# Performance work log

Hardware: AMD Instinct MI355X
Metric: run time of the kernel (lower is better)

## Reference

```python
import jax, jax.numpy as jnp
import numpy as np

N = 100000
E = 1600000
B = 64
EPS = 1e-5


def setup_inputs() -> dict:
    key = jax.random.key(0)
    ks = jax.random.split(key, 20)
    x = jax.random.normal(ks[0], (N, 3), dtype=jnp.float32)
    edge_index = jax.random.randint(ks[1], (2, E), 0, N, dtype=jnp.int64)
    batch = jnp.sort(jax.random.randint(ks[2], (N,), 0, B, dtype=jnp.int64))

    def lin(k, fan_in, fan_out):
        s = 1.0 / np.sqrt(fan_in)
        kw, kb = jax.random.split(k)
        W = jax.random.uniform(kw, (fan_in, fan_out), minval=-s, maxval=s, dtype=jnp.float32)
        b = jax.random.uniform(kb, (fan_out,), minval=-s, maxval=s, dtype=jnp.float32)
        return W, b

    W1, b1 = lin(ks[3], 3, 16)
    W2, b2 = lin(ks[4], 16, 32)
    W3, b3 = lin(ks[5], 32, 64)
    fcW, fcb = lin(ks[6], 64, 10)
    g1 = jnp.ones((16,), jnp.float32); be1 = jnp.zeros((16,), jnp.float32)
    g2 = jnp.ones((32,), jnp.float32); be2 = jnp.zeros((32,), jnp.float32)
    g3 = jnp.ones((64,), jnp.float32); be3 = jnp.zeros((64,), jnp.float32)
    return {"x": x, "edge_index": edge_index, "batch": batch,
            "W1": W1, "b1": b1, "g1": g1, "be1": be1,
            "W2": W2, "b2": b2, "g2": g2, "be2": be2,
            "W3": W3, "b3": b3, "g3": g3, "be3": be3,
            "fcW": fcW, "fcb": fcb}


def _gcn_conv(x, W, b, row, col, deg_inv_sqrt):
    # PyG GCNConv: add self-loops (pre-appended in row/col), symmetric norm,
    # scatter-add aggregation at target nodes, then bias.
    xw = x @ W                                   # [N, d_out]
    norm = deg_inv_sqrt[row] * deg_inv_sqrt[col]  # [E+N]
    msg = xw[row] * norm[:, None]                 # gather + scale
    out = jax.ops.segment_sum(msg, col, num_segments=N)
    return out + b


def _bn_relu(x, gamma, beta):
    mean = jnp.mean(x, axis=0)
    var = jnp.mean(jnp.square(x - mean), axis=0)  # biased var (torch BN)
    xh = (x - mean) * jax.lax.rsqrt(var + EPS)
    return jax.nn.relu(xh * gamma + beta)


def reference(x, edge_index, batch, W1, b1, g1, be1, W2, b2, g2, be2,
              W3, b3, g3, be3, fcW, fcb):
    loops = jnp.arange(N, dtype=edge_index.dtype)
    row = jnp.concatenate([edge_index[0], loops])
    col = jnp.concatenate([edge_index[1], loops])
    deg = jax.ops.segment_sum(jnp.ones_like(col, dtype=x.dtype), col, num_segments=N)
    dis = jax.lax.rsqrt(deg)  # deg >= 1 due to self-loops

    h = _bn_relu(_gcn_conv(x, W1, b1, row, col, dis), g1, be1)
    h = _bn_relu(_gcn_conv(h, W2, b2, row, col, dis), g2, be2)
    h = _bn_relu(_gcn_conv(h, W3, b3, row, col, dis), g3, be3)

    sums = jax.ops.segment_sum(h, batch, num_segments=B)          # [B, 64]
    cnts = jax.ops.segment_sum(jnp.ones((N,), h.dtype), batch, num_segments=B)
    pooled = sums / jnp.maximum(cnts, 1.0)[:, None]
    return pooled @ fcW + fcb                                     # [B, 10]
```

## Files before the change

### kernel.cpp

```cpp
#include <hip/hip_runtime.h>

#define N_NODES 100000
#define N_EDGES 1600000
#define B_GRAPHS 64
#define BN_EPS 1e-5
#define NBMAX 3200

#define NBUCK 256
#define BUCK_NODES 392
#define PART_CHUNK 4096
#define NB_PART 391

#define QSCALE 2048.0f
#define QINV   4.8828125e-4f

typedef _Float16 half4_t __attribute__((ext_vector_type(4)));
typedef short short4_t __attribute__((ext_vector_type(4)));
typedef int intv2 __attribute__((ext_vector_type(2)));
typedef int intv4 __attribute__((ext_vector_type(4)));
typedef float floatv4 __attribute__((ext_vector_type(4)));

static inline int cdiv(long long a, int b) { return (int)((a + b - 1) / b); }

__device__ __forceinline__ short q16(float v) {
    int q = __float2int_rn(v * QSCALE);
    q = q > 32767 ? 32767 : (q < -32768 ? -32768 : q);
    return (short)q;
}

__global__ void part_hist_kernel(const int* __restrict__ col, int* __restrict__ bucket_cnt) {
    __shared__ int h[NBUCK];
    for (int i = threadIdx.x; i < NBUCK; i += 256) h[i] = 0;
    __syncthreads();
    long long ebase = (long long)blockIdx.x * PART_CHUNK;
    int n = (N_EDGES - ebase < PART_CHUNK) ? (int)(N_EDGES - ebase) : PART_CHUNK;
    for (int i = threadIdx.x; i < n; i += 256)
        atomicAdd(&h[col[ebase + i] / BUCK_NODES], 1);
    __syncthreads();
    for (int i = threadIdx.x; i < NBUCK; i += 256)
        if (h[i]) atomicAdd(&bucket_cnt[i], h[i]);
}

__global__ void part_scan_kernel(const int* __restrict__ bucket_cnt, int* __restrict__ bucket_base,
                                 int* __restrict__ bucket_cur) {
    __shared__ int s[NBUCK];
    int t = threadIdx.x;
    int v = bucket_cnt[t];
    s[t] = v;
    __syncthreads();
    for (int off = 1; off < NBUCK; off <<= 1) {
        int u = (t >= off) ? s[t - off] : 0;
        __syncthreads();
        s[t] += u;
        __syncthreads();
    }
    bucket_base[t] = s[t] - v;
    bucket_cur[t] = s[t] - v;
}

__global__ void part_scatter_kernel(const int* __restrict__ row, const int* __restrict__ col,
                                    int* __restrict__ bucket_cur, unsigned* __restrict__ part_edges) {
    __shared__ int h[NBUCK];
    __shared__ int base_s[NBUCK];
    __shared__ int cur_s[NBUCK];
    long long ebase = (long long)blockIdx.x * PART_CHUNK;
    int n = (N_EDGES - ebase < PART_CHUNK) ? (int)(N_EDGES - ebase) : PART_CHUNK;
    for (int i = threadIdx.x; i < NBUCK; i += 256) h[i] = 0;
    __syncthreads();
    for (int i = threadIdx.x; i < n; i += 256)
        atomicAdd(&h[col[ebase + i] / BUCK_NODES], 1);
    __syncthreads();
    for (int i = threadIdx.x; i < NBUCK; i += 256) {
        int c = h[i];
        base_s[i] = c ? atomicAdd(&bucket_cur[i], c) : 0;
        cur_s[i] = 0;
    }
    __syncthreads();
    for (int i = threadIdx.x; i < n; i += 256) {
        int r = row[ebase + i], c = col[ebase + i];
        int bkt = c / BUCK_NODES;
        int p = base_s[bkt] + atomicAdd(&cur_s[bkt], 1);
        part_edges[p] = ((unsigned)r << 9) | (unsigned)(c - bkt * BUCK_NODES);
    }
}

__global__ void csr_build_kernel(const int* __restrict__ bucket_base, const unsigned* __restrict__ part_edges,
                                 int* __restrict__ row_ptr, int* __restrict__ deg,
                                 float* __restrict__ dis, int* __restrict__ sorted_row,
                                 const float* __restrict__ x, short* __restrict__ xs4) {
    __shared__ int hist[BUCK_NODES];
    __shared__ int tsum[256];
    int b = blockIdx.x;
    int t = threadIdx.x;
    int nbase = b * BUCK_NODES;
    int ebase = bucket_base[b];
    int eend = (b == NBUCK - 1) ? N_EDGES : bucket_base[b + 1];
    int ne = eend - ebase;
    for (int i = t; i < BUCK_NODES; i += 256) hist[i] = 0;
    __syncthreads();
    for (int i = t; i < ne; i += 256)
        atomicAdd(&hist[part_edges[ebase + i] & 511u], 1);
    __syncthreads();
    int a0 = 0, a1 = 0;
    if (t < BUCK_NODES / 2) { a0 = hist[2 * t]; a1 = hist[2 * t + 1]; tsum[t] = a0 + a1; }
    else tsum[t] = 0;
    __syncthreads();
    for (int off = 1; off < 256; off <<= 1) {
        int u = (t >= off) ? tsum[t - off] : 0;
        __syncthreads();
        tsum[t] += u;
        __syncthreads();
    }
    if (t < BUCK_NODES / 2) {
        int excl = tsum[t] - (a0 + a1);
        hist[2 * t] = excl;
        hist[2 * t + 1] = excl + a0;
        int n0 = nbase + 2 * t, n1 = n0 + 1;
        if (n0 < N_NODES) {
            row_ptr[n0] = ebase + excl;
            deg[n0] = a0;
            dis[n0] = rsqrtf((float)a0 + 1.0f);
        }
        if (n1 < N_NODES) {
            row_ptr[n1] = ebase + excl + a0;
            deg[n1] = a1;
            dis[n1] = rsqrtf((float)a1 + 1.0f);
        }
    }
    __syncthreads();
    for (int i = t; i < ne; i += 256) {
        unsigned e = part_edges[ebase + i];
        int p = atomicAdd(&hist[e & 511u], 1);
        sorted_row[ebase + p] = (int)(e >> 9);
    }
    for (int i = t; i < BUCK_NODES; i += 256) {
        int n = nbase + i;
        if (n < N_NODES) {
            float d = dis[n];
            short4_t v;
            v.x = q16(x[n * 3 + 0] * d);
            v.y = q16(x[n * 3 + 1] * d);
            v.z = q16(x[n * 3 + 2] * d);
            v.w = 0;
            ((short4_t*)xs4)[n] = v;
        }
    }
}

template <int WPL> struct VecSel;
template <> struct VecSel<2> { using type = intv2; };
template <> struct VecSel<4> { using type = intv4; };

template <int IN, int OUT, int INSTRIDE, int WPL>
__global__ void gather_mm_kernel(const int* __restrict__ row_ptr, const int* __restrict__ deg,
                                 const int* __restrict__ sorted_row, const float* __restrict__ dis,
                                 const short* __restrict__ hs, const float* __restrict__ W,
                                 const float* __restrict__ b, _Float16* __restrict__ pre,
                                 double* __restrict__ part_s, double* __restrict__ part_q) {
    using V = typename VecSel<WPL>::type;
    const int FPL = 2 * WPL;
    const int LPN = INSTRIDE / FPL;
    const int NPW = 64 / LPN;
    const int NPB = 4 * NPW;
    const int UNROLL = (WPL == 4) ? 4 : 8;
    __shared__ __align__(16) float lds_agg[NPB * INSTRIDE];
    __shared__ double s_s[256];
    __shared__ double s_q[256];
    int tid = threadIdx.x;
    int wv = tid >> 6, lane = tid & 63;
    int jn = wv * NPW + lane / LPN;
    int p = lane % LPN;
    int n = blockIdx.x * NPB + jn;
    if (n < N_NODES) {
        int start = row_ptr[n];
        int d = deg[n];
        const int* sr = sorted_row + start;
        const V* hv = (const V*)hs;
        V v = hv[n * LPN + p];
        int acc[FPL];
#pragma unroll
        for (int w = 0; w < WPL; w++) {
            acc[2 * w] = (int)(short)v[w];
            acc[2 * w + 1] = v[w] >> 16;
        }
        int j = 0;
        for (; j + UNROLL <= d; j += UNROLL) {
            V a[UNROLL];
#pragma unroll
            for (int u = 0; u < UNROLL; u++) a[u] = hv[sr[j + u] * LPN + p];
#pragma unroll
            for (int u = 0; u < UNROLL; u++) {
#pragma unroll
                for (int w = 0; w < WPL; w++) {
                    acc[2 * w] += (int)(short)a[u][w];
                    acc[2 * w + 1] += a[u][w] >> 16;
                }
            }
        }
        for (; j < d; j++) {
            V a = hv[sr[j] * LPN + p];
#pragma unroll
            for (int w = 0; w < WPL; w++) {
                acc[2 * w] += (int)(short)a[w];
                acc[2 * w + 1] += a[w] >> 16;
            }
        }
        float dn = dis[n] * QINV;
        float* dst = &lds_agg[(jn * LPN + p) * FPL];
#pragma unroll
        for (int k = 0; k < FPL; k++) dst[k] = dn * (float)acc[k];
    }
    __syncthreads();

    const int NG = 256 / OUT;
    int o = tid % OUT;
    int g = tid / OUT;
    float wreg[IN];
#pragma unroll
    for (int k = 0; k < IN; k++) wreg[k] = W[k * OUT + o];
    float bo = b[o];
    double my_s = 0.0, my_q = 0.0;
    for (int j2 = g; j2 < NPB; j2 += NG) {
        int nn = blockIdx.x * NPB + j2;
        if (nn < N_NODES) {
            float acc = bo;
            const floatv4* src = (const floatv4*)&lds_agg[j2 * INSTRIDE];
#pragma unroll
            for (int q = 0; q < INSTRIDE / 4; q++) {
                floatv4 vq = src[q];
#pragma unroll
                for (int c = 0; c < 4; c++) {
                    if (4 * q + c < IN) acc += vq[c] * wreg[4 * q + c];
                }
            }
            _Float16 hq = (_Float16)acc;
            pre[nn * OUT + o] = hq;
            float fq = (float)hq;
            my_s += (double)fq;
            my_q += (double)fq * (double)fq;
        }
    }
    s_s[tid] = my_s;
    s_q[tid] = my_q;
    __syncthreads();
    if (tid < OUT) {
        double ts = 0.0, tq = 0.0;
        for (int k = tid; k < 256; k += OUT) { ts += s_s[k]; tq += s_q[k]; }
        part_s[(long long)tid * NBMAX + blockIdx.x] = ts;
        part_q[(long long)tid * NBMAX + blockIdx.x] = tq;
    }
}

__global__ void bn_finalize_kernel(const double* __restrict__ part_s, const double* __restrict__ part_q,
                                   int nb, float* __restrict__ bn_mean, float* __restrict__ bn_rstd) {
    __shared__ double s_s[256];
    __shared__ double s_q[256];
    int o = blockIdx.x;
    int t = threadIdx.x;
    double ms = 0.0, mq = 0.0;
    for (int k = t; k < nb; k += 256) {
        ms += part_s[(long long)o * NBMAX + k];
        mq += part_q[(long long)o * NBMAX + k];
    }
    s_s[t] = ms;
    s_q[t] = mq;
    __syncthreads();
    for (int off = 128; off > 0; off >>= 1) {
        if (t < off) { s_s[t] += s_s[t + off]; s_q[t] += s_q[t + off]; }
        __syncthreads();
    }
    if (t == 0) {
        double mean = s_s[0] / (double)N_NODES;
        double var = s_q[0] / (double)N_NODES - mean * mean;
        bn_mean[o] = (float)mean;
        bn_rstd[o] = (float)(1.0 / sqrt(var + BN_EPS));
    }
}

template <int F>
__global__ void bn_relu_kernel(const _Float16* __restrict__ pre, const float* __restrict__ bn_mean,
                               const float* __restrict__ bn_rstd, const float* __restrict__ g,
                               const float* __restrict__ be, const float* __restrict__ dis,
                               short* __restrict__ out) {
    const int GP = F / 4;
    int t = blockIdx.x * blockDim.x + threadIdx.x;
    const int total = N_NODES * GP;
    if (t >= total) return;
    int gi = t % GP;
    int f0 = gi * 4;
    half4_t v = ((const half4_t*)pre)[t];
    float d = dis[t / GP];
    short4_t o;
#pragma unroll
    for (int k = 0; k < 4; k++) {
        int f = f0 + k;
        float y = ((float)v[k] - bn_mean[f]) * bn_rstd[f] * g[f] + be[f];
        y = y > 0.f ? y : 0.f;
        o[k] = q16(y * d);
    }
    ((short4_t*)out)[t] = o;
}

#define POOL_CHUNK 32
__global__ void pool_kernel(const _Float16* __restrict__ pre, const int* __restrict__ batch,
                            const float* __restrict__ bn_mean, const float* __restrict__ bn_rstd,
                            const float* __restrict__ g, const float* __restrict__ be,
                            float* __restrict__ pooled, float* __restrict__ cnt) {
    int wave = (blockIdx.x * blockDim.x + threadIdx.x) >> 6;
    int lane = threadIdx.x & 63;
    int start = wave * POOL_CHUNK;
    if (start >= N_NODES) return;
    int end = start + POOL_CHUNK;
    if (end > N_NODES) end = N_NODES;
    float A = bn_rstd[lane] * g[lane];
    float B = be[lane] - bn_mean[lane] * A;
    int cur = batch[start];
    float acc = 0.f;
    float c = 0.f;
    int i = start;
    for (; i + 4 <= end; i += 4) {
        int b0 = batch[i], b1 = batch[i + 1], b2 = batch[i + 2], b3 = batch[i + 3];
        float v0 = fmaxf(0.f, fmaf((float)pre[(long long)i * 64 + lane], A, B));
        float v1 = fmaxf(0.f, fmaf((float)pre[(long long)(i + 1) * 64 + lane], A, B));
        float v2 = fmaxf(0.f, fmaf((float)pre[(long long)(i + 2) * 64 + lane], A, B));
        float v3 = fmaxf(0.f, fmaf((float)pre[(long long)(i + 3) * 64 + lane], A, B));
        if (b0 != cur) { atomicAdd(&pooled[cur * 64 + lane], acc); if (lane == 0) atomicAdd(&cnt[cur], c); acc = 0.f; c = 0.f; cur = b0; }
        acc += v0; c += 1.f;
        if (b1 != cur) { atomicAdd(&pooled[cur * 64 + lane], acc); if (lane == 0) atomicAdd(&cnt[cur], c); acc = 0.f; c = 0.f; cur = b1; }
        acc += v1; c += 1.f;
        if (b2 != cur) { atomicAdd(&pooled[cur * 64 + lane], acc); if (lane == 0) atomicAdd(&cnt[cur], c); acc = 0.f; c = 0.f; cur = b2; }
        acc += v2; c += 1.f;
        if (b3 != cur) { atomicAdd(&pooled[cur * 64 + lane], acc); if (lane == 0) atomicAdd(&cnt[cur], c); acc = 0.f; c = 0.f; cur = b3; }
        acc += v3; c += 1.f;
    }
    for (; i < end; i++) {
        int b = batch[i];
        if (b != cur) { atomicAdd(&pooled[cur * 64 + lane], acc); if (lane == 0) atomicAdd(&cnt[cur], c); acc = 0.f; c = 0.f; cur = b; }
        acc += fmaxf(0.f, fmaf((float)pre[(long long)i * 64 + lane], A, B)); c += 1.f;
    }
    atomicAdd(&pooled[cur * 64 + lane], acc);
    if (lane == 0) atomicAdd(&cnt[cur], c);
}

__global__ void final_kernel(const float* __restrict__ pooled, const float* __restrict__ cnt,
                             const float* __restrict__ fcW, const float* __restrict__ fcb,
                             float* __restrict__ out) {
    int t = blockIdx.x * blockDim.x + threadIdx.x;
    if (t >= B_GRAPHS * 10) return;
    int b = t / 10, j = t % 10;
    float inv = 1.0f / fmaxf(cnt[b], 1.0f);
    float acc = fcb[j];
#pragma unroll
    for (int f = 0; f < 64; f++) acc += pooled[b * 64 + f] * inv * fcW[f * 10 + j];
    out[t] = acc;
}

extern "C" void kernel_launch(void* const* d_in, const int* in_sizes, int n_in,
                              void* d_out, int out_size, void* d_ws, size_t ws_size,
                              hipStream_t stream) {
    const float* x  = (const float*)d_in[0];
    const int* ei   = (const int*)d_in[1];
    const int* batch= (const int*)d_in[2];
    const float* W1 = (const float*)d_in[3];  const float* b1 = (const float*)d_in[4];
    const float* g1 = (const float*)d_in[5];  const float* be1= (const float*)d_in[6];
    const float* W2 = (const float*)d_in[7];  const float* b2 = (const float*)d_in[8];
    const float* g2 = (const float*)d_in[9];  const float* be2= (const float*)d_in[10];
    const float* W3 = (const float*)d_in[11]; const float* b3 = (const float*)d_in[12];
    const float* g3 = (const float*)d_in[13]; const float* be3= (const float*)d_in[14];
    const float* fcW= (const float*)d_in[15]; const float* fcb= (const float*)d_in[16];
    float* out = (float*)d_out;

    const int* row = ei;
    const int* col = ei + N_EDGES;

    char* wp = (char*)d_ws;
    int*   bucket_cnt = (int*)wp;                wp += NBUCK * 4;
    float* pooled     = (float*)wp;              wp += 64 * 64 * 4;
    float* cnt        = (float*)wp;              wp += 64 * 4;
    const size_t ZERO_BYTES = NBUCK * 4 + 64 * 64 * 4 + 64 * 4;
    float* dis        = (float*)wp;              wp += N_NODES * 4;
    int*   deg_i      = (int*)wp;                wp += N_NODES * 4;
    int*   row_ptr    = (int*)wp;                wp += N_NODES * 4;
    int*   bucket_base= (int*)wp;                wp += NBUCK * 4;
    int*   bucket_cur = (int*)wp;                wp += NBUCK * 4;
    int*   sorted_row = (int*)wp;                wp += (size_t)N_EDGES * 4;
    unsigned* part_edges = (unsigned*)wp;        wp += (size_t)N_EDGES * 4;
    double* part_s    = (double*)wp;             wp += (size_t)NBMAX * 64 * 8;
    double* part_q    = (double*)wp;             wp += (size_t)NBMAX * 64 * 8;
    float* bn_mean    = (float*)wp;              wp += 64 * 4;
    float* bn_rstd    = (float*)wp;              wp += 64 * 4;
    short* xs4q       = (short*)wp;              wp += (size_t)N_NODES * 4 * 2;
    _Float16* PRE     = (_Float16*)wp;           wp += (size_t)N_NODES * 64 * 2;
    short* Hq         = (short*)wp;              wp += (size_t)N_NODES * 32 * 2;

    const int BS = 256;

    hipMemsetAsync(bucket_cnt, 0, ZERO_BYTES, stream);

    part_hist_kernel<<<NB_PART, 256, 0, stream>>>(col, bucket_cnt);
    part_scan_kernel<<<1, NBUCK, 0, stream>>>(bucket_cnt, bucket_base, bucket_cur);
    part_scatter_kernel<<<NB_PART, 256, 0, stream>>>(row, col, bucket_cur, part_edges);
    csr_build_kernel<<<NBUCK, 256, 0, stream>>>(bucket_base, part_edges, row_ptr, deg_i, dis, sorted_row, x, xs4q);

    const int NB1 = cdiv(N_NODES, 256);
    gather_mm_kernel<3, 16, 4, 2><<<NB1, 256, 0, stream>>>(
        row_ptr, deg_i, sorted_row, dis, xs4q, W1, b1, PRE, part_s, part_q);
    bn_finalize_kernel<<<16, 256, 0, stream>>>(part_s, part_q, NB1, bn_mean, bn_rstd);
    bn_relu_kernel<16><<<cdiv((long long)N_NODES * 4, BS), BS, 0, stream>>>(
        PRE, bn_mean, bn_rstd, g1, be1, dis, Hq);

    const int NB2 = cdiv(N_NODES, 128);
    gather_mm_kernel<16, 32, 16, 4><<<NB2, 256, 0, stream>>>(
        row_ptr, deg_i, sorted_row, dis, Hq, W2, b2, PRE, part_s, part_q);
    bn_finalize_kernel<<<32, 256, 0, stream>>>(part_s, part_q, NB2, bn_mean, bn_rstd);
    bn_relu_kernel<32><<<cdiv((long long)N_NODES * 8, BS), BS, 0, stream>>>(
        PRE, bn_mean, bn_rstd, g2, be2, dis, Hq);

    const int NB3 = cdiv(N_NODES, 64);
    gather_mm_kernel<32, 64, 32, 4><<<NB3, 256, 0, stream>>>(
        row_ptr, deg_i, sorted_row, dis, Hq, W3, b3, PRE, part_s, part_q);
    bn_finalize_kernel<<<64, 256, 0, stream>>>(part_s, part_q, NB3, bn_mean, bn_rstd);

    pool_kernel<<<cdiv((long long)cdiv(N_NODES, POOL_CHUNK) * 64, BS), BS, 0, stream>>>(
        PRE, batch, bn_mean, bn_rstd, g3, be3, pooled, cnt);
    final_kernel<<<1, B_GRAPHS * 10, 0, stream>>>(pooled, cnt, fcW, fcb, out);
}
```

Measured before the change: 269.8 us.

## Replace bucketed two-pass CSR build with global atomic degree count and scatter

Result: slower. 399.8 us (+48.1%).

```diff
diff --git a/kernel.cpp b/kernel.cpp
--- a/kernel.cpp
+++ b/kernel.cpp
@@ -6,10 +6,7 @@
 #define BN_EPS 1e-5
 #define NBMAX 3200
 
-#define NBUCK 256
-#define BUCK_NODES 392
-#define PART_CHUNK 4096
-#define NB_PART 391
+#define NBS 391
 
 #define QSCALE 2048.0f
 #define QINV   4.8828125e-4f
@@ -28,82 +25,53 @@
     return (short)q;
 }
 
-__global__ void part_hist_kernel(const int* __restrict__ col, int* __restrict__ bucket_cnt) {
-    __shared__ int h[NBUCK];
-    for (int i = threadIdx.x; i < NBUCK; i += 256) h[i] = 0;
-    __syncthreads();
-    long long ebase = (long long)blockIdx.x * PART_CHUNK;
-    int n = (N_EDGES - ebase < PART_CHUNK) ? (int)(N_EDGES - ebase) : PART_CHUNK;
-    for (int i = threadIdx.x; i < n; i += 256)
-        atomicAdd(&h[col[ebase + i] / BUCK_NODES], 1);
-    __syncthreads();
-    for (int i = threadIdx.x; i < NBUCK; i += 256)
-        if (h[i]) atomicAdd(&bucket_cnt[i], h[i]);
-}
-
-__global__ void part_scan_kernel(const int* __restrict__ bucket_cnt, int* __restrict__ bucket_base,
-                                 int* __restrict__ bucket_cur) {
-    __shared__ int s[NBUCK];
+__global__ void deg_hist_kernel(const int* __restrict__ col, int* __restrict__ deg) {
+    int t = blockIdx.x * blockDim.x + threadIdx.x;
+    if (t >= N_EDGES / 4) return;
+    intv4 c = ((const intv4*)col)[t];
+    atomicAdd(&deg[c[0]], 1);
+    atomicAdd(&deg[c[1]], 1);
+    atomicAdd(&deg[c[2]], 1);
+    atomicAdd(&deg[c[3]], 1);
+}
+
+__global__ void bsum_kernel(const int* __restrict__ deg, int* __restrict__ bsum) {
+    __shared__ int s[256];
+    int b = blockIdx.x, t = threadIdx.x;
+    int n = b * 256 + t;
+    s[t] = (n < N_NODES) ? deg[n] : 0;
+    __syncthreads();
+    for (int off = 128; off > 0; off >>= 1) {
+        if (t < off) s[t] += s[t + off];
+        __syncthreads();
+    }
+    if (t == 0) bsum[b] = s[0];
+}
+
+__global__ void bscan_kernel(const int* __restrict__ bsum, int* __restrict__ bbase) {
+    __shared__ int s[512];
     int t = threadIdx.x;
-    int v = bucket_cnt[t];
+    int v = (t < NBS) ? bsum[t] : 0;
     s[t] = v;
     __syncthreads();
-    for (int off = 1; off < NBUCK; off <<= 1) {
+    for (int off = 1; off < 512; off <<= 1) {
         int u = (t >= off) ? s[t - off] : 0;
         __syncthreads();
         s[t] += u;
         __syncthreads();
     }
-    bucket_base[t] = s[t] - v;
-    bucket_cur[t] = s[t] - v;
-}
-
-__global__ void part_scatter_kernel(const int* __restrict__ row, const int* __restrict__ col,
-                                    int* __restrict__ bucket_cur, unsigned* __restrict__ part_edges) {
-    __shared__ int h[NBUCK];
-    __shared__ int base_s[NBUCK];
-    __shared__ int cur_s[NBUCK];
-    long long ebase = (long long)blockIdx.x * PART_CHUNK;
-    int n = (N_EDGES - ebase < PART_CHUNK) ? (int)(N_EDGES - ebase) : PART_CHUNK;
-    for (int i = threadIdx.x; i < NBUCK; i += 256) h[i] = 0;
-    __syncthreads();
-    for (int i = threadIdx.x; i < n; i += 256)
-        atomicAdd(&h[col[ebase + i] / BUCK_NODES], 1);
-    __syncthreads();
-    for (int i = threadIdx.x; i < NBUCK; i += 256) {
-        int c = h[i];
-        base_s[i] = c ? atomicAdd(&bucket_cur[i], c) : 0;
-        cur_s[i] = 0;
-    }
-    __syncthreads();
-    for (int i = threadIdx.x; i < n; i += 256) {
-        int r = row[ebase + i], c = col[ebase + i];
-        int bkt = c / BUCK_NODES;
-        int p = base_s[bkt] + atomicAdd(&cur_s[bkt], 1);
-        part_edges[p] = ((unsigned)r << 9) | (unsigned)(c - bkt * BUCK_NODES);
-    }
-}
-
-__global__ void csr_build_kernel(const int* __restrict__ bucket_base, const unsigned* __restrict__ part_edges,
-                                 int* __restrict__ row_ptr, int* __restrict__ deg,
-                                 float* __restrict__ dis, int* __restrict__ sorted_row,
-                                 const float* __restrict__ x, short* __restrict__ xs4) {
-    __shared__ int hist[BUCK_NODES];
+    if (t < NBS) bbase[t] = s[t] - v;
+}
+
+__global__ void csr_apply_kernel(const int* __restrict__ deg, const int* __restrict__ bbase,
+                                 int* __restrict__ row_ptr, int* __restrict__ cursor,
+                                 float* __restrict__ dis, const float* __restrict__ x,
+                                 short* __restrict__ xs4) {
     __shared__ int tsum[256];
-    int b = blockIdx.x;
-    int t = threadIdx.x;
-    int nbase = b * BUCK_NODES;
-    int ebase = bucket_base[b];
-    int eend = (b == NBUCK - 1) ? N_EDGES : bucket_base[b + 1];
-    int ne = eend - ebase;
-    for (int i = t; i < BUCK_NODES; i += 256) hist[i] = 0;
-    __syncthreads();
-    for (int i = t; i < ne; i += 256)
-        atomicAdd(&hist[part_edges[ebase + i] & 511u], 1);
-    __syncthreads();
-    int a0 = 0, a1 = 0;
-    if (t < BUCK_NODES / 2) { a0 = hist[2 * t]; a1 = hist[2 * t + 1]; tsum[t] = a0 + a1; }
-    else tsum[t] = 0;
+    int b = blockIdx.x, t = threadIdx.x;
+    int n = b * 256 + t;
+    int v = (n < N_NODES) ? deg[n] : 0;
+    tsum[t] = v;
     __syncthreads();
     for (int off = 1; off < 256; off <<= 1) {
         int u = (t >= off) ? tsum[t - off] : 0;
@@ -111,39 +79,31 @@
         tsum[t] += u;
         __syncthreads();
     }
-    if (t < BUCK_NODES / 2) {
-        int excl = tsum[t] - (a0 + a1);
-        hist[2 * t] = excl;
-        hist[2 * t + 1] = excl + a0;
-        int n0 = nbase + 2 * t, n1 = n0 + 1;
-        if (n0 < N_NODES) {
-            row_ptr[n0] = ebase + excl;
-            deg[n0] = a0;
-            dis[n0] = rsqrtf((float)a0 + 1.0f);
-        }
-        if (n1 < N_NODES) {
-            row_ptr[n1] = ebase + excl + a0;
-            deg[n1] = a1;
-            dis[n1] = rsqrtf((float)a1 + 1.0f);
-        }
-    }
-    __syncthreads();
-    for (int i = t; i < ne; i += 256) {
-        unsigned e = part_edges[ebase + i];
-        int p = atomicAdd(&hist[e & 511u], 1);
-        sorted_row[ebase + p] = (int)(e >> 9);
-    }
-    for (int i = t; i < BUCK_NODES; i += 256) {
-        int n = nbase + i;
-        if (n < N_NODES) {
-            float d = dis[n];
-            short4_t v;
-            v.x = q16(x[n * 3 + 0] * d);
-            v.y = q16(x[n * 3 + 1] * d);
-            v.z = q16(x[n * 3 + 2] * d);
-            v.w = 0;
-            ((short4_t*)xs4)[n] = v;
-        }
+    if (n < N_NODES) {
+        int rp = bbase[b] + tsum[t] - v;
+        row_ptr[n] = rp;
+        cursor[n] = rp;
+        float d = rsqrtf((float)v + 1.0f);
+        dis[n] = d;
+        short4_t q;
+        q.x = q16(x[n * 3 + 0] * d);
+        q.y = q16(x[n * 3 + 1] * d);
+        q.z = q16(x[n * 3 + 2] * d);
+        q.w = 0;
+        ((short4_t*)xs4)[n] = q;
+    }
+}
+
+__global__ void scatter_kernel(const int* __restrict__ row, const int* __restrict__ col,
+                               int* __restrict__ cursor, int* __restrict__ sorted_row) {
+    int t = blockIdx.x * blockDim.x + threadIdx.x;
+    if (t >= N_EDGES / 4) return;
+    intv4 r = ((const intv4*)row)[t];
+    intv4 c = ((const intv4*)col)[t];
+#pragma unroll
+    for (int k = 0; k < 4; k++) {
+        int p = atomicAdd(&cursor[c[k]], 1);
+        sorted_row[p] = r[k];
     }
 }
 
@@ -374,17 +334,16 @@
     const int* col = ei + N_EDGES;
 
     char* wp = (char*)d_ws;
-    int*   bucket_cnt = (int*)wp;                wp += NBUCK * 4;
+    int*   deg_i      = (int*)wp;                wp += (size_t)N_NODES * 4;
     float* pooled     = (float*)wp;              wp += 64 * 64 * 4;
     float* cnt        = (float*)wp;              wp += 64 * 4;
-    const size_t ZERO_BYTES = NBUCK * 4 + 64 * 64 * 4 + 64 * 4;
+    const size_t ZERO_BYTES = (size_t)N_NODES * 4 + 64 * 64 * 4 + 64 * 4;
     float* dis        = (float*)wp;              wp += N_NODES * 4;
-    int*   deg_i      = (int*)wp;                wp += N_NODES * 4;
     int*   row_ptr    = (int*)wp;                wp += N_NODES * 4;
-    int*   bucket_base= (int*)wp;                wp += NBUCK * 4;
-    int*   bucket_cur = (int*)wp;                wp += NBUCK * 4;
+    int*   cursor     = (int*)wp;                wp += N_NODES * 4;
+    int*   bsum       = (int*)wp;                wp += 512 * 4;
+    int*   bbase      = (int*)wp;                wp += 512 * 4;
     int*   sorted_row = (int*)wp;                wp += (size_t)N_EDGES * 4;
-    unsigned* part_edges = (unsigned*)wp;        wp += (size_t)N_EDGES * 4;
     double* part_s    = (double*)wp;             wp += (size_t)NBMAX * 64 * 8;
     double* part_q    = (double*)wp;             wp += (size_t)NBMAX * 64 * 8;
     float* bn_mean    = (float*)wp;              wp += 64 * 4;
@@ -395,12 +354,13 @@
 
     const int BS = 256;
 
-    hipMemsetAsync(bucket_cnt, 0, ZERO_BYTES, stream);
-
-    part_hist_kernel<<<NB_PART, 256, 0, stream>>>(col, bucket_cnt);
-    part_scan_kernel<<<1, NBUCK, 0, stream>>>(bucket_cnt, bucket_base, bucket_cur);
-    part_scatter_kernel<<<NB_PART, 256, 0, stream>>>(row, col, bucket_cur, part_edges);
-    csr_build_kernel<<<NBUCK, 256, 0, stream>>>(bucket_base, part_edges, row_ptr, deg_i, dis, sorted_row, x, xs4q);
+    hipMemsetAsync(deg_i, 0, ZERO_BYTES, stream);
+
+    deg_hist_kernel<<<cdiv(N_EDGES / 4, BS), BS, 0, stream>>>(col, deg_i);
+    bsum_kernel<<<NBS, 256, 0, stream>>>(deg_i, bsum);
+    bscan_kernel<<<1, 512, 0, stream>>>(bsum, bbase);
+    csr_apply_kernel<<<NBS, 256, 0, stream>>>(deg_i, bbase, row_ptr, cursor, dis, x, xs4q);
+    scatter_kernel<<<cdiv(N_EDGES / 4, BS), BS, 0, stream>>>(row, col, cursor, sorted_row);
 
     const int NB1 = cdiv(N_NODES, 256);
     gather_mm_kernel<3, 16, 4, 2><<<NB1, 256, 0, stream>>>(
```
